# Kernel tuning notes

Measured on AMD Instinct MI355X. Metric: run time of the kernel, lower is better.

The kernel has to match this reference:

```python
import jax, jax.numpy as jnp
import numpy as np

B, NSEQ, SEQ_PER = 2, 4, 256
S = NSEQ * SEQ_PER            # total sequence (stocks interleaved along seq dim)
D, H, HD = 1024, 16, 64       # d_model, nhead, head_dim
HD2, HD4 = HD // 2, HD // 4
DFF = 4096
LAMBDA_INIT = 0.2             # lambda_init_fn(0) = 0.8 - 0.6*exp(0)
SCALING = 1.0 / float(np.sqrt(HD2))
EPS_DEF = float(np.finfo(np.float32).eps)   # torch RMSNorm default eps (eps=None)
EPS_ATTN = 1e-5


def _rms(x, w, eps):
    return x * jax.lax.rsqrt(jnp.mean(x * x, axis=-1, keepdims=True) + eps) * w


def _rope(x, fc):
    # x: (B, T, NSEQ, 2H, HD2); fc: (T, HD4, 2) holding (cos, sin)
    xr = x.reshape(x.shape[:-1] + (HD4, 2))
    c = fc[None, :, None, None, :, 0]
    s = fc[None, :, None, None, :, 1]
    x0, x1 = xr[..., 0], xr[..., 1]
    return jnp.stack([x0 * c - x1 * s, x0 * s + x1 * c], axis=-1).reshape(x.shape)


def setup_inputs():
    key = jax.random.key(0)
    ks = jax.random.split(key, 16)
    def w(i, shape, std=0.02):
        return jax.random.normal(ks[i], shape, jnp.float32) * std
    # true RoPE table for seq_per_stock-1 positions
    t = jnp.arange(SEQ_PER - 1, dtype=jnp.float32)[:, None]
    inv = 1.0 / (10000.0 ** (jnp.arange(HD4, dtype=jnp.float32) / HD4))
    ang = t * inv[None, :]
    return {
        "x": jax.random.normal(ks[0], (B, S, D), jnp.float32),
        "freqs_cis": jnp.stack([jnp.cos(ang), jnp.sin(ang)], axis=-1),
        "w_norm1": jnp.ones((D,), jnp.float32),
        "w_norm2": jnp.ones((D,), jnp.float32),
        "Wq": w(1, (H * HD, D)), "bq": jnp.zeros((H * HD,), jnp.float32),
        "Wk": w(2, (H * HD, D)), "bk": jnp.zeros((H * HD,), jnp.float32),
        "Wv": w(3, (H * HD, D)), "bv": jnp.zeros((H * HD,), jnp.float32),
        "Wo": w(4, (D, H * HD)), "bo": jnp.zeros((D,), jnp.float32),
        "lq1": w(5, (HD2,), 0.1), "lk1": w(6, (HD2,), 0.1),
        "lq2": w(7, (HD2,), 0.1), "lk2": w(8, (HD2,), 0.1),
        "w_attn_norm": jnp.ones((HD,), jnp.float32),
        "Wg": w(9, (2 * DFF, D)), "bg": jnp.zeros((2 * DFF,), jnp.float32),
        "Wout": w(10, (D, DFF)), "bout": jnp.zeros((D,), jnp.float32),
    }


def reference(x, freqs_cis, w_norm1, w_norm2, Wq, bq, Wk, bk, Wv, bv, Wo, bo,
              lq1, lk1, lq2, lk2, w_attn_norm, Wg, bg, Wout, bout):
    Bz, Sz, _ = x.shape
    h = _rms(x, w_norm1, EPS_DEF)
    q = (h @ Wq.T + bq).reshape(Bz, SEQ_PER, NSEQ, 2 * H, HD2)
    k = (h @ Wk.T + bk).reshape(Bz, SEQ_PER, NSEQ, 2 * H, HD2)
    v = (h @ Wv.T + bv).reshape(Bz, Sz, H, HD).transpose(0, 2, 1, 3)   # (B,H,S,HD), interleaved order
    # RoPE on all but the first per-stock timestep; same freqs for every stock
    q = jnp.concatenate([q[:, :1], _rope(q[:, 1:], freqs_cis)], axis=1)
    k = jnp.concatenate([k[:, :1], _rope(k[:, 1:], freqs_cis)], axis=1)
    # reorder q/k to stock-major flat sequence (torch permute(0,4,1,2,3)+reshape)
    q = q.transpose(0, 2, 1, 3, 4).reshape(Bz, Sz, 2 * H, HD2).transpose(0, 2, 1, 3)
    k = k.transpose(0, 2, 1, 3, 4).reshape(Bz, Sz, 2 * H, HD2).transpose(0, 2, 1, 3)
    scores = jnp.einsum('bhqd,bhkd->bhqk', q, k) * SCALING              # (B,2H,S,S)
    causal = jnp.triu(jnp.ones((SEQ_PER, SEQ_PER), bool), 1)
    mask = jnp.tile(causal, (NSEQ, NSEQ))   # block-tiled causal, as torch .repeat
    att = jnp.sign(scores) * jax.nn.softmax(
        jnp.where(mask, -1e30, jnp.abs(scores)), axis=-1)
    lam = jnp.exp(jnp.sum(lk1 * lq1)) - jnp.exp(jnp.sum(lk2 * lq2)) + LAMBDA_INIT
    att = att.reshape(Bz, H, 2, Sz, Sz)
    a1, a2 = att[:, :, 0], att[:, :, 1]
    G = jnp.mean(a1, axis=-2, keepdims=True)          # mean over queries, broadcast back
    a = jnp.where(mask, 0.0, a1 - lam * a2 + lam * G)
    ao = jnp.einsum('bhqk,bhkd->bhqd', a, v)          # v kept in interleaved order (faithful to source)
    ao = _rms(ao, w_attn_norm, EPS_ATTN)
    ao = ao.reshape(Bz, Sz, H * HD)  # flat reinterpret (B,H,S,HD)->(B,S,H*HD), matches torch reshape chain
    x = x + ao @ Wo.T + bo
    h2 = _rms(x, w_norm2, EPS_DEF)
    u, vg = jnp.split(h2 @ Wg.T + bg, 2, axis=-1)
    return x + (u * jax.nn.silu(vg)) @ Wout.T + bout
```

## Files before the change

kernel.cpp:

```cpp
#include <hip/hip_runtime.h>

#define LAMBDA_INIT 0.2f
#define SCALING 0.17677669529663687f
#define EPS_DEF 1.1920928955078125e-07f
#define EPS_ATTN 1e-5f

typedef unsigned short us4 __attribute__((ext_vector_type(4)));
typedef unsigned short us8v __attribute__((ext_vector_type(8)));
typedef float f32x4 __attribute__((ext_vector_type(4)));
typedef float f32x2 __attribute__((ext_vector_type(2)));
typedef __bf16 bf16x8 __attribute__((ext_vector_type(8)));

#define MFMA16(a, b, c) __builtin_amdgcn_mfma_f32_16x16x32_bf16((a), (b), (c), 0, 0, 0)

__device__ __forceinline__ float bf2f(unsigned short u) {
    unsigned int x = ((unsigned int)u) << 16;
    return __builtin_bit_cast(float, x);
}
__device__ __forceinline__ unsigned short f2bf(float f) {
    unsigned int x = __builtin_bit_cast(unsigned int, f);
    x += 0x7fffu + ((x >> 16) & 1u);
    return (unsigned short)(x >> 16);
}
__device__ __forceinline__ void split8(f32x4 a, f32x4 b, us8v& hi, us8v& lo) {
#pragma unroll
    for (int u = 0; u < 4; u++) {
        unsigned short h = f2bf(a[u]);
        hi[u] = h; lo[u] = f2bf(a[u] - bf2f(h));
        unsigned short h2 = f2bf(b[u]);
        hi[4 + u] = h2; lo[4 + u] = f2bf(b[u] - bf2f(h2));
    }
}
__device__ __forceinline__ bf16x8 ldb(const unsigned short* p) {
    return __builtin_bit_cast(bf16x8, *(const us8v*)p);
}

__device__ __forceinline__ float wave_sum(float v) {
#pragma unroll
    for (int o = 32; o > 0; o >>= 1) v += __shfl_down(v, o);
    return v;
}
__device__ __forceinline__ float block_sum(float v, float* red4) {
    int wv = threadIdx.x >> 6;
    float w = wave_sum(v);
    __syncthreads();
    if ((threadIdx.x & 63) == 0) red4[wv] = w;
    __syncthreads();
    return red4[0] + red4[1] + red4[2] + red4[3];
}

__global__ __launch_bounds__(256) void prep(float* __restrict__ G, float* __restrict__ lamp,
                                            const float* lq1, const float* lk1,
                                            const float* lq2, const float* lk2) {
    int i = (blockIdx.x * 256 + threadIdx.x) * 4;
    G[i] = 0.f; G[i + 1] = 0.f; G[i + 2] = 0.f; G[i + 3] = 0.f;
    if (blockIdx.x == 0 && threadIdx.x == 0) {
        float a = 0.f, c = 0.f;
        for (int d = 0; d < 32; d++) {
            a += lq1[d] * lk1[d];
            c += lq2[d] * lk2[d];
        }
        *lamp = expf(a) - expf(c) + LAMBDA_INIT;
    }
}

template <int OUTBF>
__global__ __launch_bounds__(256) void rms_kernel(const float* __restrict__ x,
                                                  const float* __restrict__ w,
                                                  void* __restrict__ out, float eps) {
    int row = blockIdx.x;
    int tid = threadIdx.x;
    size_t base = (size_t)row * 1024 + tid * 4;
    f32x4 v = *(const f32x4*)(x + base);
    float ss = v[0]*v[0] + v[1]*v[1] + v[2]*v[2] + v[3]*v[3];
    __shared__ float red4[4];
    float tot = block_sum(ss, red4);
    float r = rsqrtf(tot * (1.0f / 1024.f) + eps);
    f32x4 wv = *(const f32x4*)(w + tid * 4);
    if (OUTBF) {
        us4 o;
#pragma unroll
        for (int i = 0; i < 4; i++) o[i] = f2bf(v[i] * r * wv[i]);
        *(us4*)((unsigned short*)out + base) = o;
    } else {
        f32x4 o;
#pragma unroll
        for (int i = 0; i < 4; i++) o[i] = v[i] * r * wv[i];
        *(f32x4*)((float*)out + base) = o;
    }
}

__global__ __launch_bounds__(256) void gemm_qkv_split(const float* __restrict__ A,
        const float* __restrict__ Wq, const float* __restrict__ Wk, const float* __restrict__ Wv,
        const float* __restrict__ bq, const float* __restrict__ bk, const float* __restrict__ bv,
        float* __restrict__ Yq, float* __restrict__ Yk, float* __restrict__ Yv) {
    const int z = blockIdx.z;
    const float* Bt  = (z == 0) ? Wq : (z == 1) ? Wk : Wv;
    const float* bias= (z == 0) ? bq : (z == 1) ? bk : bv;
    float* out       = (z == 0) ? Yq : (z == 1) ? Yk : Yv;
    const int K = 1024, N = 1024;
    __shared__ __align__(16) unsigned short Ah[64][40];
    __shared__ __align__(16) unsigned short Al[64][40];
    __shared__ __align__(16) unsigned short Bh[64][40];
    __shared__ __align__(16) unsigned short Bl[64][40];
    const int t = threadIdx.x;
    const int bm = blockIdx.x, bn = blockIdx.y;
    const int lane = t & 63, w = t >> 6;
    const int wr = w >> 1, wc = w & 1;
    const int l15 = lane & 15, lg = lane >> 4;
    const int sr = t >> 2, sc = (t & 3) * 8;

    const float* Ag = A + (size_t)(bm * 64 + sr) * K + sc;
    const float* Bg = Bt + (size_t)(bn * 64 + sr) * K + sc;

    f32x4 acc[2][2] = {};

    for (int k0 = 0; k0 < K; k0 += 32) {
        us8v ah, al, bh, bl;
        split8(*(const f32x4*)(Ag + k0), *(const f32x4*)(Ag + k0 + 4), ah, al);
        split8(*(const f32x4*)(Bg + k0), *(const f32x4*)(Bg + k0 + 4), bh, bl);
        __syncthreads();
        *(us8v*)&Ah[sr][sc] = ah;
        *(us8v*)&Al[sr][sc] = al;
        *(us8v*)&Bh[sr][sc] = bh;
        *(us8v*)&Bl[sr][sc] = bl;
        __syncthreads();
        bf16x8 afh[2], afl[2], bfh[2], bfl[2];
#pragma unroll
        for (int mi = 0; mi < 2; mi++) {
            afh[mi] = ldb(&Ah[wr * 32 + mi * 16 + l15][lg * 8]);
            afl[mi] = ldb(&Al[wr * 32 + mi * 16 + l15][lg * 8]);
        }
#pragma unroll
        for (int ni = 0; ni < 2; ni++) {
            bfh[ni] = ldb(&Bh[wc * 32 + ni * 16 + l15][lg * 8]);
            bfl[ni] = ldb(&Bl[wc * 32 + ni * 16 + l15][lg * 8]);
        }
#pragma unroll
        for (int mi = 0; mi < 2; mi++)
#pragma unroll
            for (int ni = 0; ni < 2; ni++) {
                acc[mi][ni] = MFMA16(afl[mi], bfh[ni], acc[mi][ni]);
                acc[mi][ni] = MFMA16(afh[mi], bfl[ni], acc[mi][ni]);
                acc[mi][ni] = MFMA16(afh[mi], bfh[ni], acc[mi][ni]);
            }
    }

    const int rbase = bm * 64 + wr * 32 + (lg << 2);
    const int cbase = bn * 64 + wc * 32 + l15;
#pragma unroll
    for (int mi = 0; mi < 2; mi++) {
#pragma unroll
        for (int ni = 0; ni < 2; ni++) {
            int col = cbase + ni * 16;
            float bb = bias[col];
#pragma unroll
            for (int r = 0; r < 4; r++) {
                int row = rbase + mi * 16 + r;
                out[(size_t)row * N + col] = acc[mi][ni][r] + bb;
            }
        }
    }
}

__global__ __launch_bounds__(256) void gemm_mfma(const unsigned short* __restrict__ A,
                                                 const float* __restrict__ Bt,
                                                 const float* __restrict__ bias,
                                                 const float* __restrict__ res,
                                                 float* __restrict__ out,
                                                 int M, int N, int K) {
    __shared__ __align__(16) unsigned short As[64][72];
    __shared__ __align__(16) unsigned short Bs[64][72];
    const int t = threadIdx.x;
    const int bm = blockIdx.x, bn = blockIdx.y;
    const int lane = t & 63, w = t >> 6;
    const int wr = w >> 1, wc = w & 1;
    const int l15 = lane & 15, lg = lane >> 4;
    const int sr = t >> 2, sc = (t & 3) * 16;

    const unsigned short* Ag = A + (size_t)(bm * 64 + sr) * K + sc;
    const float* Bg = Bt + (size_t)(bn * 64 + sr) * K + sc;

    f32x4 acc[2][2] = {};

    for (int k0 = 0; k0 < K; k0 += 64) {
        us8v a0 = *(const us8v*)(Ag + k0);
        us8v a1 = *(const us8v*)(Ag + k0 + 8);
        f32x4 b0 = *(const f32x4*)(Bg + k0);
        f32x4 b1 = *(const f32x4*)(Bg + k0 + 4);
        f32x4 b2 = *(const f32x4*)(Bg + k0 + 8);
        f32x4 b3 = *(const f32x4*)(Bg + k0 + 12);
        us8v bw0, bw1;
#pragma unroll
        for (int u = 0; u < 4; u++) {
            bw0[u] = f2bf(b0[u]); bw0[4 + u] = f2bf(b1[u]);
            bw1[u] = f2bf(b2[u]); bw1[4 + u] = f2bf(b3[u]);
        }
        __syncthreads();
        *(us8v*)&As[sr][sc]     = a0;
        *(us8v*)&As[sr][sc + 8] = a1;
        *(us8v*)&Bs[sr][sc]     = bw0;
        *(us8v*)&Bs[sr][sc + 8] = bw1;
        __syncthreads();
#pragma unroll
        for (int kk = 0; kk < 2; kk++) {
            bf16x8 af[2], bf[2];
#pragma unroll
            for (int mi = 0; mi < 2; mi++)
                af[mi] = ldb(&As[wr * 32 + mi * 16 + l15][kk * 32 + lg * 8]);
#pragma unroll
            for (int ni = 0; ni < 2; ni++)
                bf[ni] = ldb(&Bs[wc * 32 + ni * 16 + l15][kk * 32 + lg * 8]);
#pragma unroll
            for (int mi = 0; mi < 2; mi++)
#pragma unroll
                for (int ni = 0; ni < 2; ni++)
                    acc[mi][ni] = MFMA16(af[mi], bf[ni], acc[mi][ni]);
        }
    }

    const int rbase = bm * 64 + wr * 32 + (lg << 2);
    const int cbase = bn * 64 + wc * 32 + l15;
#pragma unroll
    for (int mi = 0; mi < 2; mi++) {
#pragma unroll
        for (int ni = 0; ni < 2; ni++) {
            int col = cbase + ni * 16;
            float bb = bias[col];
#pragma unroll
            for (int r = 0; r < 4; r++) {
                int row = rbase + mi * 16 + r;
                size_t oi = (size_t)row * N + col;
                out[oi] = acc[mi][ni][r] + bb + res[oi];
            }
        }
    }
}

__global__ __launch_bounds__(256) void gemm_gate_mfma(const unsigned short* __restrict__ A,
                                                      const float* __restrict__ Wg,
                                                      const float* __restrict__ bg,
                                                      unsigned short* __restrict__ mlp) {
    __shared__ __align__(16) unsigned short As[128][72];
    __shared__ __align__(16) unsigned short BsU[64][72];
    __shared__ __align__(16) unsigned short BsV[64][72];
    const int t = threadIdx.x;
    const int bm = blockIdx.x, bn = blockIdx.y;
    const int lane = t & 63, w = t >> 6;
    const int wr = w >> 1, wc = w & 1;
    const int l15 = lane & 15, lg = lane >> 4;
    const int sr = t >> 2, sc = (t & 3) * 16;

    const unsigned short* Ag  = A + (size_t)(bm * 128 + sr) * 1024 + sc;
    const unsigned short* Ag2 = Ag + (size_t)64 * 1024;
    const float* BgU = Wg + (size_t)(bn * 64 + sr) * 1024 + sc;
    const float* BgV = Wg + (size_t)(4096 + bn * 64 + sr) * 1024 + sc;

    f32x4 accU[4][2] = {};
    f32x4 accV[4][2] = {};

    for (int k0 = 0; k0 < 1024; k0 += 64) {
        us8v a0 = *(const us8v*)(Ag + k0);
        us8v a1 = *(const us8v*)(Ag + k0 + 8);
        us8v a2 = *(const us8v*)(Ag2 + k0);
        us8v a3 = *(const us8v*)(Ag2 + k0 + 8);
        f32x4 u0 = *(const f32x4*)(BgU + k0);
        f32x4 u1 = *(const f32x4*)(BgU + k0 + 4);
        f32x4 u2 = *(const f32x4*)(BgU + k0 + 8);
        f32x4 u3 = *(const f32x4*)(BgU + k0 + 12);
        f32x4 v0 = *(const f32x4*)(BgV + k0);
        f32x4 v1 = *(const f32x4*)(BgV + k0 + 4);
        f32x4 v2 = *(const f32x4*)(BgV + k0 + 8);
        f32x4 v3 = *(const f32x4*)(BgV + k0 + 12);
        us8v uw0, uw1, vw0, vw1;
#pragma unroll
        for (int u = 0; u < 4; u++) {
            uw0[u] = f2bf(u0[u]); uw0[4 + u] = f2bf(u1[u]);
            uw1[u] = f2bf(u2[u]); uw1[4 + u] = f2bf(u3[u]);
            vw0[u] = f2bf(v0[u]); vw0[4 + u] = f2bf(v1[u]);
            vw1[u] = f2bf(v2[u]); vw1[4 + u] = f2bf(v3[u]);
        }
        __syncthreads();
        *(us8v*)&As[sr][sc]          = a0;
        *(us8v*)&As[sr][sc + 8]      = a1;
        *(us8v*)&As[sr + 64][sc]     = a2;
        *(us8v*)&As[sr + 64][sc + 8] = a3;
        *(us8v*)&BsU[sr][sc]         = uw0;
        *(us8v*)&BsU[sr][sc + 8]     = uw1;
        *(us8v*)&BsV[sr][sc]         = vw0;
        *(us8v*)&BsV[sr][sc + 8]     = vw1;
        __syncthreads();
#pragma unroll
        for (int kk = 0; kk < 2; kk++) {
            bf16x8 af[4], bu[2], bv2[2];
#pragma unroll
            for (int mi = 0; mi < 4; mi++)
                af[mi] = ldb(&As[wr * 64 + mi * 16 + l15][kk * 32 + lg * 8]);
#pragma unroll
            for (int ni = 0; ni < 2; ni++) {
                bu[ni]  = ldb(&BsU[wc * 32 + ni * 16 + l15][kk * 32 + lg * 8]);
                bv2[ni] = ldb(&BsV[wc * 32 + ni * 16 + l15][kk * 32 + lg * 8]);
            }
#pragma unroll
            for (int mi = 0; mi < 4; mi++)
#pragma unroll
                for (int ni = 0; ni < 2; ni++) {
                    accU[mi][ni] = MFMA16(af[mi], bu[ni], accU[mi][ni]);
                    accV[mi][ni] = MFMA16(af[mi], bv2[ni], accV[mi][ni]);
                }
        }
    }

    const int rbase = bm * 128 + wr * 64 + (lg << 2);
    const int cbase = bn * 64 + wc * 32 + l15;
#pragma unroll
    for (int mi = 0; mi < 4; mi++) {
#pragma unroll
        for (int ni = 0; ni < 2; ni++) {
            int col = cbase + ni * 16;
            float bu_ = bg[col], bv_ = bg[4096 + col];
#pragma unroll
            for (int r = 0; r < 4; r++) {
                int row = rbase + mi * 16 + r;
                float u = accU[mi][ni][r] + bu_;
                float v = accV[mi][ni][r] + bv_;
                float s = v / (1.f + __expf(-v));
                mlp[(size_t)row * 4096 + col] = f2bf(u * s);
            }
        }
    }
}

__global__ __launch_bounds__(256) void rope_inplace(float* __restrict__ Y,
                                                    const float* __restrict__ fc) {
    int t = blockIdx.x;
    int s = t & 1023;
    int p = s >> 2;
    if (p == 0) return;
    int c0 = threadIdx.x * 4;
    float* y = Y + (size_t)t * 1024 + c0;
    int d4 = (c0 & 31) >> 1;
    f32x4 f = *(const f32x4*)(fc + ((size_t)(p - 1) * 16 + d4) * 2);
    float v0 = y[0], v1 = y[1], v2 = y[2], v3 = y[3];
    y[0] = v0 * f[0] - v1 * f[1];
    y[1] = v0 * f[1] + v1 * f[0];
    y[2] = v2 * f[2] - v3 * f[3];
    y[3] = v2 * f[3] + v3 * f[2];
}

__global__ __launch_bounds__(256) void pass_1(const float* __restrict__ Yq,
                                              const float* __restrict__ Yk,
                                              const float* __restrict__ Yv,
                                              const float* __restrict__ lamp,
                                              float* __restrict__ G,
                                              float* __restrict__ AOp) {
    const int blk = blockIdx.x;
    const int qc = 15 - (blk >> 5);
    const int h  = blk & 15;
    const int b  = (blk >> 4) & 1;
    const int t = threadIdx.x;
    const int lane = t & 63, w = t >> 6;
    const int l15 = lane & 15, lg = lane >> 4;

    __shared__ __align__(16) unsigned short Kh[64][72];
    __shared__ __align__(16) unsigned short Kl[64][72];
    __shared__ __align__(16) unsigned short Vth[64][72];
    __shared__ __align__(16) unsigned short Vtl[64][72];
    __shared__ __align__(16) unsigned short Wh[64][72];
    __shared__ __align__(16) unsigned short Wl[64][72];
    __shared__ float Gacc[1024];

    for (int i = t; i < 1024; i += 256) Gacc[i] = 0.f;

    us8v qh[2], ql[2];
    {
        const float* qp = Yq + ((size_t)(b * 1024 + qc * 64 + w * 16 + l15) << 10)
                          + h * 64 + lg * 8;
#pragma unroll
        for (int H = 0; H < 2; H++)
            split8(*(const f32x4*)(qp + H * 32), *(const f32x4*)(qp + H * 32 + 4), qh[H], ql[H]);
    }
    const int dq0 = w * 16 + (lg << 2);

    const float* Ykb = Yk + ((size_t)b << 20) + h * 64;
    const float* Yvb = Yv + ((size_t)b << 20) + h * 64;
    const int srow = t >> 2, ssub = t & 3;

    float z1r[4] = {0.f, 0.f, 0.f, 0.f};
    float z2r[4] = {0.f, 0.f, 0.f, 0.f};

    for (int kc = 0; kc <= qc; kc++) {
        __syncthreads();
        {
            const float* kp = Ykb + ((size_t)(kc * 64 + srow) << 10) + ssub * 16;
            us8v h0, l0, h1, l1;
            split8(*(const f32x4*)kp,       *(const f32x4*)(kp + 4),  h0, l0);
            split8(*(const f32x4*)(kp + 8), *(const f32x4*)(kp + 12), h1, l1);
            *(us8v*)&Kh[srow][ssub * 16]     = h0;
            *(us8v*)&Kh[srow][ssub * 16 + 8] = h1;
            *(us8v*)&Kl[srow][ssub * 16]     = l0;
            *(us8v*)&Kl[srow][ssub * 16 + 8] = l1;
        }
        __syncthreads();
#pragma unroll
        for (int kf = 0; kf < 4; kf++) {
            const int krow = kf * 16 + l15;
            const int kcol = lg * 8;
            bf16x8 b1h = ldb(&Kh[krow][kcol]),      b1l = ldb(&Kl[krow][kcol]);
            bf16x8 b2h = ldb(&Kh[krow][32 + kcol]), b2l = ldb(&Kl[krow][32 + kcol]);
            f32x4 s1 = {}, s2 = {};
            s1 = MFMA16(__builtin_bit_cast(bf16x8, ql[0]), b1h, s1);
            s1 = MFMA16(__builtin_bit_cast(bf16x8, qh[0]), b1l, s1);
            s1 = MFMA16(__builtin_bit_cast(bf16x8, qh[0]), b1h, s1);
            s2 = MFMA16(__builtin_bit_cast(bf16x8, ql[1]), b2h, s2);
            s2 = MFMA16(__builtin_bit_cast(bf16x8, qh[1]), b2l, s2);
            s2 = MFMA16(__builtin_bit_cast(bf16x8, qh[1]), b2h, s2);
            const int kpos = (kc * 64 + kf * 16 + l15) >> 2;
#pragma unroll
            for (int r = 0; r < 4; r++) {
                int pq = (qc * 64 + dq0 + r) >> 2;
                if (kpos <= pq) {
                    z1r[r] += __expf(fabsf(s1[r] * SCALING));
                    z2r[r] += __expf(fabsf(s2[r] * SCALING));
                }
            }
        }
    }
#pragma unroll
    for (int r = 0; r < 4; r++) {
        float a = z1r[r];
        a += __shfl_xor(a, 1); a += __shfl_xor(a, 2);
        a += __shfl_xor(a, 4); a += __shfl_xor(a, 8);
        z1r[r] = 1.f / fmaxf(a, 1e-20f);
        float c = z2r[r];
        c += __shfl_xor(c, 1); c += __shfl_xor(c, 2);
        c += __shfl_xor(c, 4); c += __shfl_xor(c, 8);
        z2r[r] = 1.f / fmaxf(c, 1e-20f);
    }
    const float lam = *lamp;

    f32x4 ao[4] = {};

    for (int kc = 0; kc <= qc; kc++) {
        __syncthreads();
        {
            const float* kp = Ykb + ((size_t)(kc * 64 + srow) << 10) + ssub * 16;
            us8v h0, l0, h1, l1;
            split8(*(const f32x4*)kp,       *(const f32x4*)(kp + 4),  h0, l0);
            split8(*(const f32x4*)(kp + 8), *(const f32x4*)(kp + 12), h1, l1);
            *(us8v*)&Kh[srow][ssub * 16]     = h0;
            *(us8v*)&Kh[srow][ssub * 16 + 8] = h1;
            *(us8v*)&Kl[srow][ssub * 16]     = l0;
            *(us8v*)&Kl[srow][ssub * 16 + 8] = l1;
            const int jv = ((srow & 3) << 8) + kc * 16 + (srow >> 2);
            const float* vp = Yvb + ((size_t)jv << 10) + ssub * 16;
            f32x4 vv[4];
            vv[0] = *(const f32x4*)vp;       vv[1] = *(const f32x4*)(vp + 4);
            vv[2] = *(const f32x4*)(vp + 8); vv[3] = *(const f32x4*)(vp + 12);
#pragma unroll
            for (int j = 0; j < 16; j++) {
                float val = vv[j >> 2][j & 3];
                unsigned short hh = f2bf(val);
                Vth[ssub * 16 + j][srow] = hh;
                Vtl[ssub * 16 + j][srow] = f2bf(val - bf2f(hh));
            }
        }
        __syncthreads();
#pragma unroll
        for (int kf = 0; kf < 4; kf++) {
            const int krow = kf * 16 + l15;
            const int kcol = lg * 8;
            bf16x8 b1h = ldb(&Kh[krow][kcol]),      b1l = ldb(&Kl[krow][kcol]);
            bf16x8 b2h = ldb(&Kh[krow][32 + kcol]), b2l = ldb(&Kl[krow][32 + kcol]);
            f32x4 s1 = {}, s2 = {};
            s1 = MFMA16(__builtin_bit_cast(bf16x8, ql[0]), b1h, s1);
            s1 = MFMA16(__builtin_bit_cast(bf16x8, qh[0]), b1l, s1);
            s1 = MFMA16(__builtin_bit_cast(bf16x8, qh[0]), b1h, s1);
            s2 = MFMA16(__builtin_bit_cast(bf16x8, ql[1]), b2h, s2);
            s2 = MFMA16(__builtin_bit_cast(bf16x8, qh[1]), b2l, s2);
            s2 = MFMA16(__builtin_bit_cast(bf16x8, qh[1]), b2h, s2);
            const int kli = kf * 16 + l15;
            const int kpos = (kc * 64 + kli) >> 2;
            float colsum = 0.f;
#pragma unroll
            for (int r = 0; r < 4; r++) {
                int pq = (qc * 64 + dq0 + r) >> 2;
                float wv = 0.f, a1 = 0.f;
                if (kpos <= pq) {
                    float t1 = s1[r] * SCALING, t2 = s2[r] * SCALING;
                    float sg1 = (t1 > 0.f) ? 1.f : ((t1 < 0.f) ? -1.f : 0.f);
                    float sg2 = (t2 > 0.f) ? 1.f : ((t2 < 0.f) ? -1.f : 0.f);
                    a1 = sg1 * __expf(fabsf(t1)) * z1r[r];
                    wv = a1 - lam * (sg2 * __expf(fabsf(t2)) * z2r[r]);
                }
                colsum += a1;
                unsigned short hh = f2bf(wv);
                Wh[dq0 + r][kli] = hh;
                Wl[dq0 + r][kli] = f2bf(wv - bf2f(hh));
            }
            colsum += __shfl_xor(colsum, 16);
            colsum += __shfl_xor(colsum, 32);
            if (lane < 16) atomicAdd(&Gacc[kc * 64 + kf * 16 + lane], colsum);
        }
        __syncthreads();
#pragma unroll
        for (int kh2 = 0; kh2 < 2; kh2++) {
            bf16x8 wah = ldb(&Wh[w * 16 + l15][kh2 * 32 + lg * 8]);
            bf16x8 wal = ldb(&Wl[w * 16 + l15][kh2 * 32 + lg * 8]);
#pragma unroll
            for (int df = 0; df < 4; df++) {
                bf16x8 vbh = ldb(&Vth[df * 16 + l15][kh2 * 32 + lg * 8]);
                bf16x8 vbl = ldb(&Vtl[df * 16 + l15][kh2 * 32 + lg * 8]);
                ao[df] = MFMA16(wah, vbl, ao[df]);
                ao[df] = MFMA16(wal, vbh, ao[df]);
                ao[df] = MFMA16(wah, vbh, ao[df]);
            }
        }
    }

#pragma unroll
    for (int df = 0; df < 4; df++) {
#pragma unroll
        for (int r = 0; r < 4; r++) {
            int tq = qc * 64 + dq0 + r;
            int qrow = ((tq & 3) << 8) + (tq >> 2);
            AOp[((((size_t)(b * 16 + h)) << 10) + qrow) * 64 + df * 16 + l15] = ao[df][r];
        }
    }

    __syncthreads();
    float* Gb = G + ((size_t)(b * 16 + h) << 10);
    const int lim = (qc + 1) << 6;
    for (int idx = t; idx < lim; idx += 256) {
        int j = ((idx & 3) << 8) + (idx >> 2);
        atomicAdd(&Gb[j], Gacc[idx]);
    }
}

__global__ __launch_bounds__(256) void pass_2a(const float* __restrict__ G,
                                               const float* __restrict__ Yv,
                                               float* __restrict__ GVpre) {
    const int h = blockIdx.x, b = blockIdx.y;
    const int t = threadIdx.x;
    __shared__ float Gl[1024];
    __shared__ float S[256][64];
    __shared__ float segsum[4][64];
    for (int i = t; i < 1024; i += 256) Gl[i] = G[((size_t)(b * 16 + h) << 10) + i];
    __syncthreads();
    const int d = t & 63, pg = t >> 6;
    const float* Yvb = Yv + ((size_t)b << 20) + h * 64 + d;
    for (int p0 = 0; p0 < 64; p0++) {
        int pos = pg * 64 + p0;
        float s = 0.f;
#pragma unroll
        for (int sq = 0; sq < 4; sq++) {
            int j = (sq << 8) + pos;
            s += Gl[j] * Yvb[(size_t)j << 10];
        }
        S[pos][d] = s;
    }
    __syncthreads();
    float acc = 0.f;
    for (int p0 = 0; p0 < 64; p0++) {
        int pos = pg * 64 + p0;
        acc += S[pos][d];
        S[pos][d] = acc;
    }
    segsum[pg][d] = acc;
    __syncthreads();
    float off = 0.f;
    for (int g = 0; g < pg; g++) off += segsum[g][d];
    float* gv = GVpre + (((size_t)(b * 16 + h)) << 14) + d;
    for (int p0 = 0; p0 < 64; p0++) {
        int pos = pg * 64 + p0;
        gv[pos << 6] = S[pos][d] + off;
    }
}

__global__ __launch_bounds__(256) void pass_2b(const float* __restrict__ AOp,
                                               const float* __restrict__ GVpre,
                                               const float* __restrict__ lamp,
                                               const float* __restrict__ wan,
                                               unsigned short* __restrict__ aoS) {
    const int qg = blockIdx.x;
    const int h = blockIdx.y, b = blockIdx.z;
    const int t = threadIdx.x;
    const int d = t & 63, rg = t >> 6;
    const float lamg = (*lamp) * (1.f / 1024.f);
    const float wv = wan[d];
    const float* aob = AOp + ((((size_t)(b * 16 + h)) << 10) + (qg << 8)) * 64 + d;
    const float* gvb = GVpre + (((size_t)(b * 16 + h)) << 14) + d;
    unsigned short* ob = aoS + ((size_t)b << 20) + ((size_t)h << 16) + ((size_t)(qg << 8) << 6) + d;
    for (int p0 = 0; p0 < 64; p0++) {
        int pq = p0 * 4 + rg;
        float ao = aob[(size_t)pq << 6] + lamg * gvb[(size_t)pq << 6];
        float ss = ao * ao;
#pragma unroll
        for (int o = 1; o < 64; o <<= 1) ss += __shfl_xor(ss, o);
        float rr_ = rsqrtf(ss * (1.f / 64.f) + EPS_ATTN);
        ob[(size_t)pq << 6] = f2bf(ao * rr_ * wv);
    }
}

extern "C" void kernel_launch(void* const* d_in, const int* in_sizes, int n_in,
                              void* d_out, int out_size, void* d_ws, size_t ws_size,
                              hipStream_t stream) {
    const float* x    = (const float*)d_in[0];
    const float* fc   = (const float*)d_in[1];
    const float* w1   = (const float*)d_in[2];
    const float* w2   = (const float*)d_in[3];
    const float* Wq   = (const float*)d_in[4];
    const float* bq   = (const float*)d_in[5];
    const float* Wk   = (const float*)d_in[6];
    const float* bk   = (const float*)d_in[7];
    const float* Wv   = (const float*)d_in[8];
    const float* bv   = (const float*)d_in[9];
    const float* Wo   = (const float*)d_in[10];
    const float* bo   = (const float*)d_in[11];
    const float* lq1  = (const float*)d_in[12];
    const float* lk1  = (const float*)d_in[13];
    const float* lq2  = (const float*)d_in[14];
    const float* lk2  = (const float*)d_in[15];
    const float* wan  = (const float*)d_in[16];
    const float* Wg   = (const float*)d_in[17];
    const float* bg   = (const float*)d_in[18];
    const float* Wout = (const float*)d_in[19];
    const float* bout = (const float*)d_in[20];

    char* ws = (char*)d_ws;
    const size_t MB = 1024 * 1024;
    float* G    = (float*)(ws);
    float* lam  = (float*)(ws + 256 * 1024);
    float* h32  = (float*)(ws + 1 * MB);
    float* Yq   = (float*)(ws + 9 * MB);
    float* Yk   = (float*)(ws + 17 * MB);
    float* Yv   = (float*)(ws + 25 * MB);
    float* AOp  = (float*)(ws + 33 * MB);
    float* GVpre= (float*)(ws + 41 * MB);
    unsigned short* aoS = (unsigned short*)(ws + 1 * MB);
    float* X1           = (float*)(ws + 9 * MB);
    unsigned short* h2b = (unsigned short*)(ws + 1 * MB);
    unsigned short* mlp = (unsigned short*)(ws + 17 * MB);

    prep<<<32, 256, 0, stream>>>(G, lam, lq1, lk1, lq2, lk2);
    rms_kernel<0><<<2048, 256, 0, stream>>>(x, w1, h32, EPS_DEF);
    gemm_qkv_split<<<dim3(32, 16, 3), 256, 0, stream>>>(h32, Wq, Wk, Wv, bq, bk, bv, Yq, Yk, Yv);
    rope_inplace<<<2048, 256, 0, stream>>>(Yq, fc);
    rope_inplace<<<2048, 256, 0, stream>>>(Yk, fc);
    pass_1<<<512, 256, 0, stream>>>(Yq, Yk, Yv, lam, G, AOp);
    pass_2a<<<dim3(16, 2), 256, 0, stream>>>(G, Yv, GVpre);
    pass_2b<<<dim3(4, 16, 2), 256, 0, stream>>>(AOp, GVpre, lam, wan, aoS);
    dim3 gmf(32, 16);
    gemm_mfma<<<gmf, 256, 0, stream>>>(aoS, Wo, bo, x, X1, 2048, 1024, 1024);
    rms_kernel<1><<<2048, 256, 0, stream>>>(X1, w2, h2b, EPS_DEF);
    gemm_gate_mfma<<<dim3(16, 64), 256, 0, stream>>>(h2b, Wg, bg, mlp);
    gemm_mfma<<<gmf, 256, 0, stream>>>(mlp, Wout, bout, X1, (float*)d_out, 2048, 1024, 4096);
}
```

Measured before the change: 503.4 us.

## Precompute bf16 hi/lo K and transposed V splits, pre-convert Wo/Wout to bf16

Adds separate kernels that do RoPE on K and write its bf16 hi/lo split in de-interleaved order, and that transpose V into bf16 hi/lo buffers per head. pass_1 then loads these directly instead of redoing the fp32-to-bf16 split and transpose for every query chunk, which was repeated work across up to 16 query blocks. Wo and Wout are converted to bf16 once per call, so the output GEMMs read half the weight bytes and skip per-tile conversion. The cost is extra launches and extra global traffic for the intermediate buffers, plus a reshuffled G accumulation index and a changed workspace layout.

```diff
diff --git a/kernel.cpp b/kernel.cpp
--- a/kernel.cpp
+++ b/kernel.cpp
@@ -62,6 +62,17 @@
         }
         *lamp = expf(a) - expf(c) + LAMBDA_INIT;
     }
+}
+
+__global__ __launch_bounds__(256) void cvt_bf16(const float* __restrict__ s,
+                                                unsigned short* __restrict__ d, int n4) {
+    int i = blockIdx.x * 256 + threadIdx.x;
+    if (i >= n4) return;
+    f32x4 v = ((const f32x4*)s)[i];
+    us4 o;
+#pragma unroll
+    for (int u = 0; u < 4; u++) o[u] = f2bf(v[u]);
+    ((us4*)d)[i] = o;
 }
 
 template <int OUTBF>
@@ -163,12 +174,12 @@
     }
 }
 
-__global__ __launch_bounds__(256) void gemm_mfma(const unsigned short* __restrict__ A,
-                                                 const float* __restrict__ Bt,
-                                                 const float* __restrict__ bias,
-                                                 const float* __restrict__ res,
-                                                 float* __restrict__ out,
-                                                 int M, int N, int K) {
+__global__ __launch_bounds__(256) void gemm_mfma_wb(const unsigned short* __restrict__ A,
+                                                    const unsigned short* __restrict__ Bt,
+                                                    const float* __restrict__ bias,
+                                                    const float* __restrict__ res,
+                                                    float* __restrict__ out,
+                                                    int M, int N, int K) {
     __shared__ __align__(16) unsigned short As[64][72];
     __shared__ __align__(16) unsigned short Bs[64][72];
     const int t = threadIdx.x;
@@ -179,28 +190,20 @@
     const int sr = t >> 2, sc = (t & 3) * 16;
 
     const unsigned short* Ag = A + (size_t)(bm * 64 + sr) * K + sc;
-    const float* Bg = Bt + (size_t)(bn * 64 + sr) * K + sc;
+    const unsigned short* Bg = Bt + (size_t)(bn * 64 + sr) * K + sc;
 
     f32x4 acc[2][2] = {};
 
     for (int k0 = 0; k0 < K; k0 += 64) {
         us8v a0 = *(const us8v*)(Ag + k0);
         us8v a1 = *(const us8v*)(Ag + k0 + 8);
-        f32x4 b0 = *(const f32x4*)(Bg + k0);
-        f32x4 b1 = *(const f32x4*)(Bg + k0 + 4);
-        f32x4 b2 = *(const f32x4*)(Bg + k0 + 8);
-        f32x4 b3 = *(const f32x4*)(Bg + k0 + 12);
-        us8v bw0, bw1;
-#pragma unroll
-        for (int u = 0; u < 4; u++) {
-            bw0[u] = f2bf(b0[u]); bw0[4 + u] = f2bf(b1[u]);
-            bw1[u] = f2bf(b2[u]); bw1[4 + u] = f2bf(b3[u]);
-        }
+        us8v b0 = *(const us8v*)(Bg + k0);
+        us8v b1 = *(const us8v*)(Bg + k0 + 8);
         __syncthreads();
         *(us8v*)&As[sr][sc]     = a0;
         *(us8v*)&As[sr][sc + 8] = a1;
-        *(us8v*)&Bs[sr][sc]     = bw0;
-        *(us8v*)&Bs[sr][sc + 8] = bw1;
+        *(us8v*)&Bs[sr][sc]     = b0;
+        *(us8v*)&Bs[sr][sc + 8] = b1;
         __syncthreads();
 #pragma unroll
         for (int kk = 0; kk < 2; kk++) {
@@ -348,9 +351,69 @@
     y[3] = v2 * f[3] + v3 * f[2];
 }
 
+__global__ __launch_bounds__(256) void rope_split_k(const float* __restrict__ Yk,
+                                                    const float* __restrict__ fc,
+                                                    unsigned short* __restrict__ KhG,
+                                                    unsigned short* __restrict__ KlG) {
+    int t = blockIdx.x;
+    int s = t & 1023;
+    int p = s >> 2;
+    int c0 = threadIdx.x * 4;
+    const float* y = Yk + (size_t)t * 1024 + c0;
+    float v0 = y[0], v1 = y[1], v2 = y[2], v3 = y[3];
+    if (p > 0) {
+        int d4 = (c0 & 31) >> 1;
+        f32x4 f = *(const f32x4*)(fc + ((size_t)(p - 1) * 16 + d4) * 2);
+        float w0 = v0 * f[0] - v1 * f[1];
+        float w1 = v0 * f[1] + v1 * f[0];
+        float w2 = v2 * f[2] - v3 * f[3];
+        float w3 = v2 * f[3] + v3 * f[2];
+        v0 = w0; v1 = w1; v2 = w2; v3 = w3;
+    }
+    us4 hi, lo;
+    hi[0] = f2bf(v0); lo[0] = f2bf(v0 - bf2f(hi[0]));
+    hi[1] = f2bf(v1); lo[1] = f2bf(v1 - bf2f(hi[1]));
+    hi[2] = f2bf(v2); lo[2] = f2bf(v2 - bf2f(hi[2]));
+    hi[3] = f2bf(v3); lo[3] = f2bf(v3 - bf2f(hi[3]));
+    *(us4*)(KhG + (size_t)t * 1024 + c0) = hi;
+    *(us4*)(KlG + (size_t)t * 1024 + c0) = lo;
+}
+
+__global__ __launch_bounds__(256) void v_split_t(const float* __restrict__ Yv,
+                                                 unsigned short* __restrict__ VtH,
+                                                 unsigned short* __restrict__ VtL) {
+    const int jc = blockIdx.x, h = blockIdx.y, b = blockIdx.z;
+    __shared__ float tile[64][65];
+    const int t = threadIdx.x;
+    {
+        const int jr = t >> 2, dc = (t & 3) * 16;
+        const float* src = Yv + ((size_t)(b * 1024 + jc * 64 + jr) << 10) + h * 64 + dc;
+        *(f32x4*)&tile[jr][dc]      = *(const f32x4*)src;
+        *(f32x4*)&tile[jr][dc + 4]  = *(const f32x4*)(src + 4);
+        *(f32x4*)&tile[jr][dc + 8]  = *(const f32x4*)(src + 8);
+        *(f32x4*)&tile[jr][dc + 12] = *(const f32x4*)(src + 12);
+    }
+    __syncthreads();
+    const int d = t >> 2, js = (t & 3) * 16;
+    us8v h0, h1, l0, l1;
+#pragma unroll
+    for (int n = 0; n < 16; n++) {
+        float val = tile[js + n][d];
+        unsigned short hh = f2bf(val);
+        unsigned short ll = f2bf(val - bf2f(hh));
+        if (n < 8) { h0[n] = hh; l0[n] = ll; }
+        else       { h1[n - 8] = hh; l1[n - 8] = ll; }
+    }
+    size_t ob = (((size_t)(b * 16 + h) * 64 + d) << 10) + jc * 64 + js;
+    *(us8v*)(VtH + ob) = h0; *(us8v*)(VtH + ob + 8) = h1;
+    *(us8v*)(VtL + ob) = l0; *(us8v*)(VtL + ob + 8) = l1;
+}
+
 __global__ __launch_bounds__(256) void pass_1(const float* __restrict__ Yq,
-                                              const float* __restrict__ Yk,
-                                              const float* __restrict__ Yv,
+                                              const unsigned short* __restrict__ KhG,
+                                              const unsigned short* __restrict__ KlG,
+                                              const unsigned short* __restrict__ VtH,
+                                              const unsigned short* __restrict__ VtL,
                                               const float* __restrict__ lamp,
                                               float* __restrict__ G,
                                               float* __restrict__ AOp) {
@@ -382,9 +445,12 @@
     }
     const int dq0 = w * 16 + (lg << 2);
 
-    const float* Ykb = Yk + ((size_t)b << 20) + h * 64;
-    const float* Yvb = Yv + ((size_t)b << 20) + h * 64;
     const int srow = t >> 2, ssub = t & 3;
+    const int ptk = 4 * (srow & 15) + (srow >> 4);
+    const unsigned short* KhB = KhG + ((size_t)(b * 1024) << 10) + h * 64;
+    const unsigned short* KlB = KlG + ((size_t)(b * 1024) << 10) + h * 64;
+    const unsigned short* VhB = VtH + (((size_t)(b * 16 + h) * 64 + srow) << 10) + ssub * 256;
+    const unsigned short* VlB = VtL + (((size_t)(b * 16 + h) * 64 + srow) << 10) + ssub * 256;
 
     float z1r[4] = {0.f, 0.f, 0.f, 0.f};
     float z2r[4] = {0.f, 0.f, 0.f, 0.f};
@@ -392,16 +458,15 @@
     for (int kc = 0; kc <= qc; kc++) {
         __syncthreads();
         {
-            const float* kp = Ykb + ((size_t)(kc * 64 + srow) << 10) + ssub * 16;
-            us8v h0, l0, h1, l1;
-            split8(*(const f32x4*)kp,       *(const f32x4*)(kp + 4),  h0, l0);
-            split8(*(const f32x4*)(kp + 8), *(const f32x4*)(kp + 12), h1, l1);
-            *(us8v*)&Kh[srow][ssub * 16]     = h0;
-            *(us8v*)&Kh[srow][ssub * 16 + 8] = h1;
-            *(us8v*)&Kl[srow][ssub * 16]     = l0;
-            *(us8v*)&Kl[srow][ssub * 16 + 8] = l1;
-        }
-        __syncthreads();
+            const unsigned short* kh = KhB + ((size_t)(kc * 64 + ptk) << 10) + ssub * 16;
+            const unsigned short* kl = KlB + ((size_t)(kc * 64 + ptk) << 10) + ssub * 16;
+            *(us8v*)&Kh[srow][ssub * 16]     = *(const us8v*)kh;
+            *(us8v*)&Kh[srow][ssub * 16 + 8] = *(const us8v*)(kh + 8);
+            *(us8v*)&Kl[srow][ssub * 16]     = *(const us8v*)kl;
+            *(us8v*)&Kl[srow][ssub * 16 + 8] = *(const us8v*)(kl + 8);
+        }
+        __syncthreads();
+        const int kpos = kc * 16 + l15;
 #pragma unroll
         for (int kf = 0; kf < 4; kf++) {
             const int krow = kf * 16 + l15;
@@ -415,7 +480,6 @@
             s2 = MFMA16(__builtin_bit_cast(bf16x8, ql[1]), b2h, s2);
             s2 = MFMA16(__builtin_bit_cast(bf16x8, qh[1]), b2l, s2);
             s2 = MFMA16(__builtin_bit_cast(bf16x8, qh[1]), b2h, s2);
-            const int kpos = (kc * 64 + kf * 16 + l15) >> 2;
 #pragma unroll
             for (int r = 0; r < 4; r++) {
                 int pq = (qc * 64 + dq0 + r) >> 2;
@@ -444,28 +508,21 @@
     for (int kc = 0; kc <= qc; kc++) {
         __syncthreads();
         {
-            const float* kp = Ykb + ((size_t)(kc * 64 + srow) << 10) + ssub * 16;
-            us8v h0, l0, h1, l1;
-            split8(*(const f32x4*)kp,       *(const f32x4*)(kp + 4),  h0, l0);
-            split8(*(const f32x4*)(kp + 8), *(const f32x4*)(kp + 12), h1, l1);
-            *(us8v*)&Kh[srow][ssub * 16]     = h0;
-            *(us8v*)&Kh[srow][ssub * 16 + 8] = h1;
-            *(us8v*)&Kl[srow][ssub * 16]     = l0;
-            *(us8v*)&Kl[srow][ssub * 16 + 8] = l1;
-            const int jv = ((srow & 3) << 8) + kc * 16 + (srow >> 2);
-            const float* vp = Yvb + ((size_t)jv << 10) + ssub * 16;
-            f32x4 vv[4];
-            vv[0] = *(const f32x4*)vp;       vv[1] = *(const f32x4*)(vp + 4);
-            vv[2] = *(const f32x4*)(vp + 8); vv[3] = *(const f32x4*)(vp + 12);
-#pragma unroll
-            for (int j = 0; j < 16; j++) {
-                float val = vv[j >> 2][j & 3];
-                unsigned short hh = f2bf(val);
-                Vth[ssub * 16 + j][srow] = hh;
-                Vtl[ssub * 16 + j][srow] = f2bf(val - bf2f(hh));
-            }
-        }
-        __syncthreads();
+            const unsigned short* kh = KhB + ((size_t)(kc * 64 + ptk) << 10) + ssub * 16;
+            const unsigned short* kl = KlB + ((size_t)(kc * 64 + ptk) << 10) + ssub * 16;
+            *(us8v*)&Kh[srow][ssub * 16]     = *(const us8v*)kh;
+            *(us8v*)&Kh[srow][ssub * 16 + 8] = *(const us8v*)(kh + 8);
+            *(us8v*)&Kl[srow][ssub * 16]     = *(const us8v*)kl;
+            *(us8v*)&Kl[srow][ssub * 16 + 8] = *(const us8v*)(kl + 8);
+            const unsigned short* vh = VhB + kc * 16;
+            const unsigned short* vl = VlB + kc * 16;
+            *(us8v*)&Vth[srow][ssub * 16]     = *(const us8v*)vh;
+            *(us8v*)&Vth[srow][ssub * 16 + 8] = *(const us8v*)(vh + 8);
+            *(us8v*)&Vtl[srow][ssub * 16]     = *(const us8v*)vl;
+            *(us8v*)&Vtl[srow][ssub * 16 + 8] = *(const us8v*)(vl + 8);
+        }
+        __syncthreads();
+        const int kpos = kc * 16 + l15;
 #pragma unroll
         for (int kf = 0; kf < 4; kf++) {
             const int krow = kf * 16 + l15;
@@ -480,7 +537,6 @@
             s2 = MFMA16(__builtin_bit_cast(bf16x8, qh[1]), b2l, s2);
             s2 = MFMA16(__builtin_bit_cast(bf16x8, qh[1]), b2h, s2);
             const int kli = kf * 16 + l15;
-            const int kpos = (kc * 64 + kli) >> 2;
             float colsum = 0.f;
 #pragma unroll
             for (int r = 0; r < 4; r++) {
@@ -500,7 +556,7 @@
             }
             colsum += __shfl_xor(colsum, 16);
             colsum += __shfl_xor(colsum, 32);
-            if (lane < 16) atomicAdd(&Gacc[kc * 64 + kf * 16 + lane], colsum);
+            if (lane < 16) atomicAdd(&Gacc[kf * 256 + kc * 16 + lane], colsum);
         }
         __syncthreads();
 #pragma unroll
@@ -530,10 +586,9 @@
 
     __syncthreads();
     float* Gb = G + ((size_t)(b * 16 + h) << 10);
-    const int lim = (qc + 1) << 6;
-    for (int idx = t; idx < lim; idx += 256) {
-        int j = ((idx & 3) << 8) + (idx >> 2);
-        atomicAdd(&Gb[j], Gacc[idx]);
+    const int limp = (qc + 1) << 4;
+    for (int idx = t; idx < 1024; idx += 256) {
+        if ((idx & 255) < limp) atomicAdd(&Gb[idx], Gacc[idx]);
     }
 }
 
@@ -637,22 +692,31 @@
     float* Yv   = (float*)(ws + 25 * MB);
     float* AOp  = (float*)(ws + 33 * MB);
     float* GVpre= (float*)(ws + 41 * MB);
+    unsigned short* WoB   = (unsigned short*)(ws + 43 * MB);
+    unsigned short* WoutB = (unsigned short*)(ws + 45 * MB);
+    unsigned short* KhG = (unsigned short*)(ws + 1 * MB);
+    unsigned short* KlG = (unsigned short*)(ws + 5 * MB);
+    unsigned short* VtH = (unsigned short*)(ws + 17 * MB);
+    unsigned short* VtL = (unsigned short*)(ws + 21 * MB);
     unsigned short* aoS = (unsigned short*)(ws + 1 * MB);
     float* X1           = (float*)(ws + 9 * MB);
-    unsigned short* h2b = (unsigned short*)(ws + 1 * MB);
+    unsigned short* h2b = (unsigned short*)(ws + 5 * MB);
     unsigned short* mlp = (unsigned short*)(ws + 17 * MB);
 
     prep<<<32, 256, 0, stream>>>(G, lam, lq1, lk1, lq2, lk2);
+    cvt_bf16<<<1024, 256, 0, stream>>>(Wo, WoB, 262144);
+    cvt_bf16<<<4096, 256, 0, stream>>>(Wout, WoutB, 1048576);
     rms_kernel<0><<<2048, 256, 0, stream>>>(x, w1, h32, EPS_DEF);
     gemm_qkv_split<<<dim3(32, 16, 3), 256, 0, stream>>>(h32, Wq, Wk, Wv, bq, bk, bv, Yq, Yk, Yv);
     rope_inplace<<<2048, 256, 0, stream>>>(Yq, fc);
-    rope_inplace<<<2048, 256, 0, stream>>>(Yk, fc);
-    pass_1<<<512, 256, 0, stream>>>(Yq, Yk, Yv, lam, G, AOp);
+    rope_split_k<<<2048, 256, 0, stream>>>(Yk, fc, KhG, KlG);
+    v_split_t<<<dim3(16, 16, 2), 256, 0, stream>>>(Yv, VtH, VtL);
+    pass_1<<<512, 256, 0, stream>>>(Yq, KhG, KlG, VtH, VtL, lam, G, AOp);
     pass_2a<<<dim3(16, 2), 256, 0, stream>>>(G, Yv, GVpre);
     pass_2b<<<dim3(4, 16, 2), 256, 0, stream>>>(AOp, GVpre, lam, wan, aoS);
     dim3 gmf(32, 16);
-    gemm_mfma<<<gmf, 256, 0, stream>>>(aoS, Wo, bo, x, X1, 2048, 1024, 1024);
+    gemm_mfma_wb<<<gmf, 256, 0, stream>>>(aoS, WoB, bo, x, X1, 2048, 1024, 1024);
     rms_kernel<1><<<2048, 256, 0, stream>>>(X1, w2, h2b, EPS_DEF);
     gemm_gate_mfma<<<dim3(16, 64), 256, 0, stream>>>(h2b, Wg, bg, mlp);
-    gemm_mfma<<<gmf, 256, 0, stream>>>(mlp, Wout, bout, X1, (float*)d_out, 2048, 1024, 4096);
-}
+    gemm_mfma_wb<<<gmf, 256, 0, stream>>>(mlp, WoutB, bout, X1, (float*)d_out, 2048, 1024, 4096);
+}
```

After: 476.2 us. 5.4% less time.
